# Kernel optimization log

Measured on AMD Instinct MI355X. Metric: run time of the kernel, lower is better.

The kernel has to match this reference:

```python
import jax, jax.numpy as jnp
import numpy as np

N_NODES = 100000
N_EDGES = 600000
F_IN, HID, CLS = 128, 128, 16


def sage_conv(x, src, dst, W_l, b_l, W_r, n_nodes):
    # mean aggregation of neighbor features: message x[src] scattered to dst
    msg = x[src]                                              # [E, F]
    agg = jax.ops.segment_sum(msg, dst, num_segments=n_nodes)  # [N, F]
    deg = jax.ops.segment_sum(jnp.ones((src.shape[0],), x.dtype), dst, num_segments=n_nodes)
    agg = agg / jnp.maximum(deg, 1.0)[:, None]
    # PyG SAGEConv: lin_l(agg) (with bias) + lin_r(x_root) (no bias)
    return agg @ W_l + b_l + x @ W_r


def setup_inputs() -> dict:
    key = jax.random.key(0)
    ks = jax.random.split(key, 6)
    x = jax.random.normal(ks[0], (N_NODES, F_IN), jnp.float32)
    edge_index = jax.random.randint(ks[1], (2, N_EDGES), 0, N_NODES, dtype=jnp.int64)
    s1 = 1.0 / np.sqrt(F_IN)
    s2 = 1.0 / np.sqrt(HID)
    return {
        "x": x,
        "edge_index": edge_index,
        "W1_l": jax.random.normal(ks[2], (F_IN, HID), jnp.float32) * s1,
        "b1": jnp.zeros((HID,), jnp.float32),
        "W1_r": jax.random.normal(ks[3], (F_IN, HID), jnp.float32) * s1,
        "W2_l": jax.random.normal(ks[4], (HID, CLS), jnp.float32) * s2,
        "b2": jnp.zeros((CLS,), jnp.float32),
        "W2_r": jax.random.normal(ks[5], (HID, CLS), jnp.float32) * s2,
    }


def reference(x, edge_index, W1_l, b1, W1_r, W2_l, b2, W2_r):
    n = x.shape[0]
    src, dst = edge_index[0], edge_index[1]
    h = sage_conv(x, src, dst, W1_l, b1, W1_r, n)
    h = jax.nn.relu(h)
    # F.dropout(training=self.training): identity in eval mode
    out = sage_conv(h, src, dst, W2_l, b2, W2_r, n)
    return jax.nn.log_softmax(out, axis=1)
```

## Files before the change

### kernel.cpp

```cpp
#include <hip/hip_runtime.h>
#include <cstdint>

#define N_NODES 100000
#define N_PAD 100096
#define N_EDGES 600000
#define F 128
#define CLS 16
#define CAP 32

typedef short bf16x8 __attribute__((ext_vector_type(8)));
typedef float f32x4 __attribute__((ext_vector_type(4)));

__device__ inline float bf2f(unsigned int lo16) { return __uint_as_float(lo16 << 16); }
__device__ inline unsigned short f2b(float f) {
    unsigned int u = __float_as_uint(f);
    return (unsigned short)((u + 0x7fffu + ((u >> 16) & 1u)) >> 16);
}

__global__ __launch_bounds__(256) void init_k(int* __restrict__ deg,
                                              const float* __restrict__ x,
                                              unsigned short* __restrict__ xb,
                                              const float* __restrict__ W1l,
                                              const float* __restrict__ W1r,
                                              const float* __restrict__ W2l,
                                              const float* __restrict__ W2r,
                                              unsigned short* __restrict__ w1t,
                                              unsigned short* __restrict__ w2t) {
    int b = blockIdx.x;
    if (b < 98) {
        int i = b * 1024 + threadIdx.x * 4;
#pragma unroll
        for (int k = 0; k < 4; k++)
            if (i + k < N_NODES) deg[i + k] = 0;
    } else if (b < 12598) {
        int i = (b - 98) * 256 + threadIdx.x;
        if (i < N_NODES * F / 4) {
            float4 v = ((const float4*)x)[i];
            ushort4 o;
            o.x = f2b(v.x); o.y = f2b(v.y); o.z = f2b(v.z); o.w = f2b(v.w);
            ((ushort4*)xb)[i] = o;
        }
    } else if (b < 12726) {
        int idx = (b - 12598) * 256 + threadIdx.x;
        int n = idx >> 8, k = idx & 255;
        float v = (k < F) ? W1l[k * F + n] : W1r[(k - F) * F + n];
        int ct = n >> 4, m = n & 15;
        int half = k >> 7, ks = (k >> 5) & 3, quad = (k >> 3) & 3, j = k & 7;
        w1t[(ct * 8 + ks * 2 + half) * 512 + (quad * 16 + m) * 8 + j] = f2b(v);
    } else {
        int idx = (b - 12726) * 256 + threadIdx.x;
        if (idx < 32 * F) {
            int n = idx >> 7, k = idx & 127;
            float v = (n < CLS) ? W2l[k * CLS + n] : W2r[k * CLS + (n - CLS)];
            int tile = n >> 4, m = n & 15;
            int ks = (k >> 5) & 3, quad = (k >> 3) & 3, j = k & 7;
            w2t[(tile * 4 + ks) * 512 + (quad * 16 + m) * 8 + j] = f2b(v);
        }
    }
}

__global__ void fill_k(const int* __restrict__ src, const int* __restrict__ dst,
                       int* __restrict__ deg, int* __restrict__ bucket) {
    int e = blockIdx.x * blockDim.x + threadIdx.x;
    if (e < N_EDGES) {
        int d = dst[e];
        int slot = atomicAdd(&deg[d], 1);
        if (slot < CAP) bucket[d * CAP + slot] = src[e];
    }
}

__global__ __launch_bounds__(256) void gemm_fused(const unsigned short* __restrict__ Xb,
                                                  const int* __restrict__ deg,
                                                  const int* __restrict__ bucket,
                                                  const unsigned short* __restrict__ Wt,
                                                  const float* __restrict__ bias,
                                                  const unsigned short* __restrict__ Wt2,
                                                  unsigned short* __restrict__ trLb,
                                                  float* __restrict__ trR) {
    __shared__ unsigned short sh[128 * 136];
    int tid = threadIdx.x;
    int row0 = blockIdx.x * 128;

    {
        int ns = tid >> 1, half = tid & 1;
        const int4* gsrc = (const int4*)(bucket + (size_t)(row0 + ns) * CAP + half * 16);
        int* drow = (int*)(sh + ns * 136);
        int4* ldst = (int4*)(drow + half * 16);
        ldst[0] = gsrc[0];
        ldst[1] = gsrc[1];
        ldst[2] = gsrc[2];
        ldst[3] = gsrc[3];
        if (half == 0) drow[32] = deg[row0 + ns];
    }

    int grp = tid >> 4, l16 = tid & 15, f8 = l16 * 8;
    int lrb = grp * 8;

#define ISSUE(P, DV, LR) do { \
    const int* brow_ = (const int*)(sh + (LR) * 136); \
    int node_ = row0 + (LR); \
    int draw_ = brow_[32]; \
    DV = (node_ < N_NODES) ? min(max(draw_, 0), CAP) : 0; \
    int4 b0_ = ((const int4*)brow_)[0]; \
    int4 b1_ = ((const int4*)brow_)[1]; \
    int4 b2_ = ((const int4*)brow_)[2]; \
    int n0_  = (DV > 0 ) ? min(max(b0_.x, 0), N_NODES - 1) : 0; \
    int n1_  = (DV > 1 ) ? min(max(b0_.y, 0), N_NODES - 1) : 0; \
    int n2_  = (DV > 2 ) ? min(max(b0_.z, 0), N_NODES - 1) : 0; \
    int n3_  = (DV > 3 ) ? min(max(b0_.w, 0), N_NODES - 1) : 0; \
    int n4_  = (DV > 4 ) ? min(max(b1_.x, 0), N_NODES - 1) : 0; \
    int n5_  = (DV > 5 ) ? min(max(b1_.y, 0), N_NODES - 1) : 0; \
    int n6_  = (DV > 6 ) ? min(max(b1_.z, 0), N_NODES - 1) : 0; \
    int n7_  = (DV > 7 ) ? min(max(b1_.w, 0), N_NODES - 1) : 0; \
    int n8_  = (DV > 8 ) ? min(max(b2_.x, 0), N_NODES - 1) : 0; \
    int n9_  = (DV > 9 ) ? min(max(b2_.y, 0), N_NODES - 1) : 0; \
    int n10_ = (DV > 10) ? min(max(b2_.z, 0), N_NODES - 1) : 0; \
    int n11_ = (DV > 11) ? min(max(b2_.w, 0), N_NODES - 1) : 0; \
    P##0  = *(const uint4*)(Xb + (size_t)n0_  * F + f8); \
    P##1  = *(const uint4*)(Xb + (size_t)n1_  * F + f8); \
    P##2  = *(const uint4*)(Xb + (size_t)n2_  * F + f8); \
    P##3  = *(const uint4*)(Xb + (size_t)n3_  * F + f8); \
    P##4  = *(const uint4*)(Xb + (size_t)n4_  * F + f8); \
    P##5  = *(const uint4*)(Xb + (size_t)n5_  * F + f8); \
    P##6  = *(const uint4*)(Xb + (size_t)n6_  * F + f8); \
    P##7  = *(const uint4*)(Xb + (size_t)n7_  * F + f8); \
    P##8  = *(const uint4*)(Xb + (size_t)n8_  * F + f8); \
    P##9  = *(const uint4*)(Xb + (size_t)n9_  * F + f8); \
    P##10 = *(const uint4*)(Xb + (size_t)n10_ * F + f8); \
    P##11 = *(const uint4*)(Xb + (size_t)n11_ * F + f8); \
} while (0)

#define ACC8(vv) { \
    acc_[0] += bf2f((vv).x & 0xffffu); acc_[1] += bf2f((vv).x >> 16); \
    acc_[2] += bf2f((vv).y & 0xffffu); acc_[3] += bf2f((vv).y >> 16); \
    acc_[4] += bf2f((vv).z & 0xffffu); acc_[5] += bf2f((vv).z >> 16); \
    acc_[6] += bf2f((vv).w & 0xffffu); acc_[7] += bf2f((vv).w >> 16); }

#define CONSUME(P, DV, LR) do { \
    float acc_[8] = {0.f, 0.f, 0.f, 0.f, 0.f, 0.f, 0.f, 0.f}; \
    if (DV > 0)  ACC8(P##0); \
    if (DV > 1)  ACC8(P##1); \
    if (DV > 2)  ACC8(P##2); \
    if (DV > 3)  ACC8(P##3); \
    if (DV > 4)  ACC8(P##4); \
    if (DV > 5)  ACC8(P##5); \
    if (DV > 6)  ACC8(P##6); \
    if (DV > 7)  ACC8(P##7); \
    if (DV > 8)  ACC8(P##8); \
    if (DV > 9)  ACC8(P##9); \
    if (DV > 10) ACC8(P##10); \
    if (DV > 11) ACC8(P##11); \
    if (DV > 12) { \
        const int* brow_ = (const int*)(sh + (LR) * 136); \
        for (int j0 = 12; j0 < DV; j0 += 4) { \
            int4 bb_ = *(const int4*)(brow_ + j0); \
            int rem_ = DV - j0; \
            int m0_ = (rem_ > 0) ? min(max(bb_.x, 0), N_NODES - 1) : 0; \
            int m1_ = (rem_ > 1) ? min(max(bb_.y, 0), N_NODES - 1) : 0; \
            int m2_ = (rem_ > 2) ? min(max(bb_.z, 0), N_NODES - 1) : 0; \
            int m3_ = (rem_ > 3) ? min(max(bb_.w, 0), N_NODES - 1) : 0; \
            uint4 w0_ = *(const uint4*)(Xb + (size_t)m0_ * F + f8); \
            uint4 w1_ = *(const uint4*)(Xb + (size_t)m1_ * F + f8); \
            uint4 w2_ = *(const uint4*)(Xb + (size_t)m2_ * F + f8); \
            uint4 w3_ = *(const uint4*)(Xb + (size_t)m3_ * F + f8); \
            if (rem_ > 0) ACC8(w0_); \
            if (rem_ > 1) ACC8(w1_); \
            if (rem_ > 2) ACC8(w2_); \
            if (rem_ > 3) ACC8(w3_); \
        } \
    } \
    float inv_ = 1.0f / fmaxf((float)DV, 1.0f); \
    uint4 o_; \
    o_.x = (unsigned int)f2b(acc_[0] * inv_) | ((unsigned int)f2b(acc_[1] * inv_) << 16); \
    o_.y = (unsigned int)f2b(acc_[2] * inv_) | ((unsigned int)f2b(acc_[3] * inv_) << 16); \
    o_.z = (unsigned int)f2b(acc_[4] * inv_) | ((unsigned int)f2b(acc_[5] * inv_) << 16); \
    o_.w = (unsigned int)f2b(acc_[6] * inv_) | ((unsigned int)f2b(acc_[7] * inv_) << 16); \
    *(uint4*)&sh[(LR) * 136 + f8] = o_; \
} while (0)

    {
        uint4 vA0, vA1, vA2, vA3, vA4, vA5, vA6, vA7, vA8, vA9, vA10, vA11;
        uint4 vB0, vB1, vB2, vB3, vB4, vB5, vB6, vB7, vB8, vB9, vB10, vB11;
        int dA, dB;
        ISSUE(vA, dA, lrb + 0);
        ISSUE(vB, dB, lrb + 1);
        CONSUME(vA, dA, lrb + 0);
        ISSUE(vA, dA, lrb + 2);
        CONSUME(vB, dB, lrb + 1);
        ISSUE(vB, dB, lrb + 3);
        CONSUME(vA, dA, lrb + 2);
        ISSUE(vA, dA, lrb + 4);
        CONSUME(vB, dB, lrb + 3);
        ISSUE(vB, dB, lrb + 5);
        CONSUME(vA, dA, lrb + 4);
        ISSUE(vA, dA, lrb + 6);
        CONSUME(vB, dB, lrb + 5);
        ISSUE(vB, dB, lrb + 7);
        CONSUME(vA, dA, lrb + 6);
        CONSUME(vB, dB, lrb + 7);
    }
#undef ISSUE
#undef ACC8
#undef CONSUME
    __syncthreads();

    int wave = tid >> 6, lane = tid & 63;
    int m = lane & 15, quad = lane >> 4;
    int koff = quad * 8;
    int wrow0 = row0 + wave * 32;

    const unsigned short* sa0 = sh + (wave * 32 + m) * 136 + koff;
    const unsigned short* sa1 = sa0 + 16 * 136;
    const unsigned short* px0 = Xb + (size_t)(wrow0 + m) * F + koff;
    const unsigned short* px1 = px0 + 16 * F;
    const unsigned short* pw = Wt + lane * 8;

    f32x4 acc0[8], acc1[8];
#pragma unroll
    for (int ct = 0; ct < 8; ct++) { acc0[ct] = (f32x4){0,0,0,0}; acc1[ct] = (f32x4){0,0,0,0}; }

#pragma unroll
    for (int ks = 0; ks < 4; ks++) {
        bf16x8 a0 = *(const bf16x8*)(const void*)(sa0 + ks * 32);
        bf16x8 a1 = *(const bf16x8*)(const void*)(sa1 + ks * 32);
        bf16x8 x0 = *(const bf16x8*)(const void*)(px0 + ks * 32);
        bf16x8 x1 = *(const bf16x8*)(const void*)(px1 + ks * 32);
#pragma unroll
        for (int ct = 0; ct < 8; ct++) {
            bf16x8 bl = *(const bf16x8*)(const void*)(pw + (ct * 8 + ks * 2 + 0) * 512);
            bf16x8 br = *(const bf16x8*)(const void*)(pw + (ct * 8 + ks * 2 + 1) * 512);
            acc0[ct] = __builtin_amdgcn_mfma_f32_16x16x32_bf16(a0, bl, acc0[ct], 0, 0, 0);
            acc1[ct] = __builtin_amdgcn_mfma_f32_16x16x32_bf16(a1, bl, acc1[ct], 0, 0, 0);
            acc0[ct] = __builtin_amdgcn_mfma_f32_16x16x32_bf16(x0, br, acc0[ct], 0, 0, 0);
            acc1[ct] = __builtin_amdgcn_mfma_f32_16x16x32_bf16(x1, br, acc1[ct], 0, 0, 0);
        }
    }
    __syncthreads();

    int lr0 = wave * 32 + quad * 4;
#pragma unroll
    for (int ct = 0; ct < 8; ct++) {
        int n = ct * 16 + m;
        float bv = bias[n];
#pragma unroll
        for (int r = 0; r < 4; r++) {
            sh[(lr0 + r) * 136 + n]      = f2b(fmaxf(acc0[ct][r] + bv, 0.f));
            sh[(lr0 + 16 + r) * 136 + n] = f2b(fmaxf(acc1[ct][r] + bv, 0.f));
        }
    }
    __syncthreads();

    const unsigned short* hl0 = sh + (wave * 32 + m) * 136 + koff;
    const unsigned short* hl1 = hl0 + 16 * 136;
    const unsigned short* pw2 = Wt2 + lane * 8;

    f32x4 al0 = (f32x4){0,0,0,0}, al1 = (f32x4){0,0,0,0};
    f32x4 ar0 = (f32x4){0,0,0,0}, ar1 = (f32x4){0,0,0,0};
#pragma unroll
    for (int ks = 0; ks < 4; ks++) {
        bf16x8 h0 = *(const bf16x8*)(const void*)(hl0 + ks * 32);
        bf16x8 h1 = *(const bf16x8*)(const void*)(hl1 + ks * 32);
        bf16x8 wl = *(const bf16x8*)(const void*)(pw2 + (0 * 4 + ks) * 512);
        bf16x8 wr = *(const bf16x8*)(const void*)(pw2 + (1 * 4 + ks) * 512);
        al0 = __builtin_amdgcn_mfma_f32_16x16x32_bf16(h0, wl, al0, 0, 0, 0);
        al1 = __builtin_amdgcn_mfma_f32_16x16x32_bf16(h1, wl, al1, 0, 0, 0);
        ar0 = __builtin_amdgcn_mfma_f32_16x16x32_bf16(h0, wr, ar0, 0, 0, 0);
        ar1 = __builtin_amdgcn_mfma_f32_16x16x32_bf16(h1, wr, ar1, 0, 0, 0);
    }
    int r0 = wrow0 + quad * 4;
#pragma unroll
    for (int r = 0; r < 4; r++) {
        trLb[(size_t)(r0 + r) * CLS + m]      = f2b(al0[r]);
        trLb[(size_t)(r0 + 16 + r) * CLS + m] = f2b(al1[r]);
        trR[(size_t)(r0 + r) * CLS + m]       = ar0[r];
        trR[(size_t)(r0 + 16 + r) * CLS + m]  = ar1[r];
    }
}

__global__ __launch_bounds__(256) void agg2sm_k(const unsigned short* __restrict__ trLb,
                                                const float* __restrict__ trR,
                                                const int* __restrict__ deg,
                                                const int* __restrict__ bucket,
                                                const float* __restrict__ b2,
                                                float* __restrict__ out) {
    int node = blockIdx.x * 4 + (threadIdx.x >> 6);
    int lane = threadIdx.x & 63;
    int r = lane >> 2;
    int cq = (lane & 3) * 4;
    const int* bk = bucket + node * CAP;

    int d_raw = deg[node];
    int d = min(d_raw, CAP);
    int nb = (r < d) ? min(max(bk[r], 0), N_NODES - 1) : 0;
    uint2 v = *(const uint2*)(trLb + (size_t)nb * CLS + cq);
    float4 selfR = *(const float4*)(trR + (size_t)node * CLS + cq);

    float4 acc = {0.f, 0.f, 0.f, 0.f};
    if (r < d) {
        acc.x += bf2f(v.x & 0xffffu); acc.y += bf2f(v.x >> 16);
        acc.z += bf2f(v.y & 0xffffu); acc.w += bf2f(v.y >> 16);
    }
    if (d > 16) {
        int idx = 16 + r;
        bool valid = idx < d;
        int m2 = valid ? min(max(bk[idx], 0), N_NODES - 1) : 0;
        uint2 w = *(const uint2*)(trLb + (size_t)m2 * CLS + cq);
        if (valid) {
            acc.x += bf2f(w.x & 0xffffu); acc.y += bf2f(w.x >> 16);
            acc.z += bf2f(w.y & 0xffffu); acc.w += bf2f(w.y >> 16);
        }
    }
#pragma unroll
    for (int off = 4; off <= 32; off <<= 1) {
        acc.x += __shfl_xor(acc.x, off);
        acc.y += __shfl_xor(acc.y, off);
        acc.z += __shfl_xor(acc.z, off);
        acc.w += __shfl_xor(acc.w, off);
    }
    float inv = 1.0f / fmaxf((float)d, 1.0f);
    float4 bb = *(const float4*)(b2 + cq);
    float vx = acc.x * inv + selfR.x + bb.x;
    float vy = acc.y * inv + selfR.y + bb.y;
    float vz = acc.z * inv + selfR.z + bb.z;
    float vw = acc.w * inv + selfR.w + bb.w;
    float mx = fmaxf(fmaxf(vx, vy), fmaxf(vz, vw));
    mx = fmaxf(mx, __shfl_xor(mx, 1));
    mx = fmaxf(mx, __shfl_xor(mx, 2));
    float sm = __expf(vx - mx) + __expf(vy - mx) + __expf(vz - mx) + __expf(vw - mx);
    sm += __shfl_xor(sm, 1);
    sm += __shfl_xor(sm, 2);
    float lg = __logf(sm);
    if (r == 0) {
        float4 o = {vx - mx - lg, vy - mx - lg, vz - mx - lg, vw - mx - lg};
        *(float4*)(out + (size_t)node * CLS + cq) = o;
    }
}


extern "C" void kernel_launch(void* const* d_in, const int* in_sizes, int n_in,
                              void* d_out, int out_size, void* d_ws, size_t ws_size,
                              hipStream_t stream) {
    const float* x   = (const float*)d_in[0];
    const int*   ei  = (const int*)d_in[1];
    const float* W1l = (const float*)d_in[2];
    const float* b1  = (const float*)d_in[3];
    const float* W1r = (const float*)d_in[4];
    const float* W2l = (const float*)d_in[5];
    const float* b2  = (const float*)d_in[6];
    const float* W2r = (const float*)d_in[7];
    float* out = (float*)d_out;

    const int* src = ei;
    const int* dst = ei + N_EDGES;

    char* ws = (char*)d_ws;
    size_t off = 0;
    auto alloc = [&](size_t bytes) { char* p = ws + off; off += (bytes + 127) / 128 * 128; return p; };
    int* deg    = (int*)alloc((size_t)N_NODES * 4);
    int* bucket = (int*)alloc((size_t)N_NODES * CAP * 4);
    unsigned short* xb   = (unsigned short*)alloc((size_t)N_PAD * F * 2);
    unsigned short* trLb = (unsigned short*)alloc((size_t)N_PAD * CLS * 2);
    float*          trR  = (float*)alloc((size_t)N_PAD * CLS * 4);
    unsigned short* w1t  = (unsigned short*)alloc((size_t)F * 256 * 2);
    unsigned short* w2t  = (unsigned short*)alloc((size_t)32 * F * 2);

    init_k<<<12743, 256, 0, stream>>>(deg, x, xb, W1l, W1r, W2l, W2r, w1t, w2t);
    fill_k<<<(N_EDGES + 255) / 256, 256, 0, stream>>>(src, dst, deg, bucket);
    gemm_fused<<<N_PAD / 128, 256, 0, stream>>>(xb, deg, bucket, w1t, b1, w2t, trLb, trR);
    agg2sm_k<<<N_NODES / 4, 256, 0, stream>>>(trLb, trR, deg, bucket, b2, out);
}
```

Measured before the change: 211.1 us.

## Fuse edge bucketing into prep kernel and narrow gather lanes to 4 features

Moves degree zeroing to a memset and merges the edge bucket-fill kernel with the bf16 conversion and weight-packing kernel, which removes one kernel launch and lets the atomics overlap with the conversion work. In the fused GEMM's neighbour-mean gather, each thread now handles 4 features with 8-byte loads instead of 8 features with 16-byte loads, so 32 threads cover a row and each group processes 16 rows in a rolled loop. This is meant to lower register pressure and raise occupancy, at the cost of more, smaller gather transactions. The x conversion branch also drops its bounds check, which relies on the block count exactly covering the array.

New measurement: 218.6 us. 3.6% more time.

```diff
diff --git a/kernel.cpp b/kernel.cpp
--- a/kernel.cpp
+++ b/kernel.cpp
@@ -17,7 +17,10 @@
     return (unsigned short)((u + 0x7fffu + ((u >> 16) & 1u)) >> 16);
 }
 
-__global__ __launch_bounds__(256) void init_k(int* __restrict__ deg,
+__global__ __launch_bounds__(256) void prep_k(const int* __restrict__ src,
+                                              const int* __restrict__ dst,
+                                              int* __restrict__ deg,
+                                              int* __restrict__ bucket,
                                               const float* __restrict__ x,
                                               unsigned short* __restrict__ xb,
                                               const float* __restrict__ W1l,
@@ -27,28 +30,28 @@
                                               unsigned short* __restrict__ w1t,
                                               unsigned short* __restrict__ w2t) {
     int b = blockIdx.x;
-    if (b < 98) {
-        int i = b * 1024 + threadIdx.x * 4;
-#pragma unroll
-        for (int k = 0; k < 4; k++)
-            if (i + k < N_NODES) deg[i + k] = 0;
-    } else if (b < 12598) {
-        int i = (b - 98) * 256 + threadIdx.x;
-        if (i < N_NODES * F / 4) {
-            float4 v = ((const float4*)x)[i];
-            ushort4 o;
-            o.x = f2b(v.x); o.y = f2b(v.y); o.z = f2b(v.z); o.w = f2b(v.w);
-            ((ushort4*)xb)[i] = o;
-        }
-    } else if (b < 12726) {
-        int idx = (b - 12598) * 256 + threadIdx.x;
+    if (b < 2344) {
+        int e = b * 256 + threadIdx.x;
+        if (e < N_EDGES) {
+            int d = dst[e];
+            int slot = atomicAdd(&deg[d], 1);
+            if (slot < CAP) bucket[d * CAP + slot] = src[e];
+        }
+    } else if (b < 14844) {
+        int i = (b - 2344) * 256 + threadIdx.x;
+        float4 v = ((const float4*)x)[i];
+        ushort4 o;
+        o.x = f2b(v.x); o.y = f2b(v.y); o.z = f2b(v.z); o.w = f2b(v.w);
+        ((ushort4*)xb)[i] = o;
+    } else if (b < 14972) {
+        int idx = (b - 14844) * 256 + threadIdx.x;
         int n = idx >> 8, k = idx & 255;
         float v = (k < F) ? W1l[k * F + n] : W1r[(k - F) * F + n];
         int ct = n >> 4, m = n & 15;
         int half = k >> 7, ks = (k >> 5) & 3, quad = (k >> 3) & 3, j = k & 7;
         w1t[(ct * 8 + ks * 2 + half) * 512 + (quad * 16 + m) * 8 + j] = f2b(v);
     } else {
-        int idx = (b - 12726) * 256 + threadIdx.x;
+        int idx = (b - 14972) * 256 + threadIdx.x;
         if (idx < 32 * F) {
             int n = idx >> 7, k = idx & 127;
             float v = (n < CLS) ? W2l[k * CLS + n] : W2r[k * CLS + (n - CLS)];
@@ -56,16 +59,6 @@
             int ks = (k >> 5) & 3, quad = (k >> 3) & 3, j = k & 7;
             w2t[(tile * 4 + ks) * 512 + (quad * 16 + m) * 8 + j] = f2b(v);
         }
-    }
-}
-
-__global__ void fill_k(const int* __restrict__ src, const int* __restrict__ dst,
-                       int* __restrict__ deg, int* __restrict__ bucket) {
-    int e = blockIdx.x * blockDim.x + threadIdx.x;
-    if (e < N_EDGES) {
-        int d = dst[e];
-        int slot = atomicAdd(&deg[d], 1);
-        if (slot < CAP) bucket[d * CAP + slot] = src[e];
     }
 }
 
@@ -93,8 +86,8 @@
         if (half == 0) drow[32] = deg[row0 + ns];
     }
 
-    int grp = tid >> 4, l16 = tid & 15, f8 = l16 * 8;
-    int lrb = grp * 8;
+    int grp = tid >> 5, c4 = (tid & 31) * 4;
+    int lrb = grp * 16;
 
 #define ISSUE(P, DV, LR) do { \
     const int* brow_ = (const int*)(sh + (LR) * 136); \
@@ -116,40 +109,38 @@
     int n9_  = (DV > 9 ) ? min(max(b2_.y, 0), N_NODES - 1) : 0; \
     int n10_ = (DV > 10) ? min(max(b2_.z, 0), N_NODES - 1) : 0; \
     int n11_ = (DV > 11) ? min(max(b2_.w, 0), N_NODES - 1) : 0; \
-    P##0  = *(const uint4*)(Xb + (size_t)n0_  * F + f8); \
-    P##1  = *(const uint4*)(Xb + (size_t)n1_  * F + f8); \
-    P##2  = *(const uint4*)(Xb + (size_t)n2_  * F + f8); \
-    P##3  = *(const uint4*)(Xb + (size_t)n3_  * F + f8); \
-    P##4  = *(const uint4*)(Xb + (size_t)n4_  * F + f8); \
-    P##5  = *(const uint4*)(Xb + (size_t)n5_  * F + f8); \
-    P##6  = *(const uint4*)(Xb + (size_t)n6_  * F + f8); \
-    P##7  = *(const uint4*)(Xb + (size_t)n7_  * F + f8); \
-    P##8  = *(const uint4*)(Xb + (size_t)n8_  * F + f8); \
-    P##9  = *(const uint4*)(Xb + (size_t)n9_  * F + f8); \
-    P##10 = *(const uint4*)(Xb + (size_t)n10_ * F + f8); \
-    P##11 = *(const uint4*)(Xb + (size_t)n11_ * F + f8); \
+    P##0  = *(const uint2*)(Xb + (size_t)n0_  * F + c4); \
+    P##1  = *(const uint2*)(Xb + (size_t)n1_  * F + c4); \
+    P##2  = *(const uint2*)(Xb + (size_t)n2_  * F + c4); \
+    P##3  = *(const uint2*)(Xb + (size_t)n3_  * F + c4); \
+    P##4  = *(const uint2*)(Xb + (size_t)n4_  * F + c4); \
+    P##5  = *(const uint2*)(Xb + (size_t)n5_  * F + c4); \
+    P##6  = *(const uint2*)(Xb + (size_t)n6_  * F + c4); \
+    P##7  = *(const uint2*)(Xb + (size_t)n7_  * F + c4); \
+    P##8  = *(const uint2*)(Xb + (size_t)n8_  * F + c4); \
+    P##9  = *(const uint2*)(Xb + (size_t)n9_  * F + c4); \
+    P##10 = *(const uint2*)(Xb + (size_t)n10_ * F + c4); \
+    P##11 = *(const uint2*)(Xb + (size_t)n11_ * F + c4); \
 } while (0)
 
-#define ACC8(vv) { \
+#define ACC4(vv) { \
     acc_[0] += bf2f((vv).x & 0xffffu); acc_[1] += bf2f((vv).x >> 16); \
-    acc_[2] += bf2f((vv).y & 0xffffu); acc_[3] += bf2f((vv).y >> 16); \
-    acc_[4] += bf2f((vv).z & 0xffffu); acc_[5] += bf2f((vv).z >> 16); \
-    acc_[6] += bf2f((vv).w & 0xffffu); acc_[7] += bf2f((vv).w >> 16); }
+    acc_[2] += bf2f((vv).y & 0xffffu); acc_[3] += bf2f((vv).y >> 16); }
 
 #define CONSUME(P, DV, LR) do { \
-    float acc_[8] = {0.f, 0.f, 0.f, 0.f, 0.f, 0.f, 0.f, 0.f}; \
-    if (DV > 0)  ACC8(P##0); \
-    if (DV > 1)  ACC8(P##1); \
-    if (DV > 2)  ACC8(P##2); \
-    if (DV > 3)  ACC8(P##3); \
-    if (DV > 4)  ACC8(P##4); \
-    if (DV > 5)  ACC8(P##5); \
-    if (DV > 6)  ACC8(P##6); \
-    if (DV > 7)  ACC8(P##7); \
-    if (DV > 8)  ACC8(P##8); \
-    if (DV > 9)  ACC8(P##9); \
-    if (DV > 10) ACC8(P##10); \
-    if (DV > 11) ACC8(P##11); \
+    float acc_[4] = {0.f, 0.f, 0.f, 0.f}; \
+    if (DV > 0)  ACC4(P##0); \
+    if (DV > 1)  ACC4(P##1); \
+    if (DV > 2)  ACC4(P##2); \
+    if (DV > 3)  ACC4(P##3); \
+    if (DV > 4)  ACC4(P##4); \
+    if (DV > 5)  ACC4(P##5); \
+    if (DV > 6)  ACC4(P##6); \
+    if (DV > 7)  ACC4(P##7); \
+    if (DV > 8)  ACC4(P##8); \
+    if (DV > 9)  ACC4(P##9); \
+    if (DV > 10) ACC4(P##10); \
+    if (DV > 11) ACC4(P##11); \
     if (DV > 12) { \
         const int* brow_ = (const int*)(sh + (LR) * 136); \
         for (int j0 = 12; j0 < DV; j0 += 4) { \
@@ -159,48 +150,41 @@
             int m1_ = (rem_ > 1) ? min(max(bb_.y, 0), N_NODES - 1) : 0; \
             int m2_ = (rem_ > 2) ? min(max(bb_.z, 0), N_NODES - 1) : 0; \
             int m3_ = (rem_ > 3) ? min(max(bb_.w, 0), N_NODES - 1) : 0; \
-            uint4 w0_ = *(const uint4*)(Xb + (size_t)m0_ * F + f8); \
-            uint4 w1_ = *(const uint4*)(Xb + (size_t)m1_ * F + f8); \
-            uint4 w2_ = *(const uint4*)(Xb + (size_t)m2_ * F + f8); \
-            uint4 w3_ = *(const uint4*)(Xb + (size_t)m3_ * F + f8); \
-            if (rem_ > 0) ACC8(w0_); \
-            if (rem_ > 1) ACC8(w1_); \
-            if (rem_ > 2) ACC8(w2_); \
-            if (rem_ > 3) ACC8(w3_); \
+            uint2 w0_ = *(const uint2*)(Xb + (size_t)m0_ * F + c4); \
+            uint2 w1_ = *(const uint2*)(Xb + (size_t)m1_ * F + c4); \
+            uint2 w2_ = *(const uint2*)(Xb + (size_t)m2_ * F + c4); \
+            uint2 w3_ = *(const uint2*)(Xb + (size_t)m3_ * F + c4); \
+            if (rem_ > 0) ACC4(w0_); \
+            if (rem_ > 1) ACC4(w1_); \
+            if (rem_ > 2) ACC4(w2_); \
+            if (rem_ > 3) ACC4(w3_); \
         } \
     } \
     float inv_ = 1.0f / fmaxf((float)DV, 1.0f); \
-    uint4 o_; \
+    uint2 o_; \
     o_.x = (unsigned int)f2b(acc_[0] * inv_) | ((unsigned int)f2b(acc_[1] * inv_) << 16); \
     o_.y = (unsigned int)f2b(acc_[2] * inv_) | ((unsigned int)f2b(acc_[3] * inv_) << 16); \
-    o_.z = (unsigned int)f2b(acc_[4] * inv_) | ((unsigned int)f2b(acc_[5] * inv_) << 16); \
-    o_.w = (unsigned int)f2b(acc_[6] * inv_) | ((unsigned int)f2b(acc_[7] * inv_) << 16); \
-    *(uint4*)&sh[(LR) * 136 + f8] = o_; \
+    *(uint2*)&sh[(LR) * 136 + c4] = o_; \
 } while (0)
 
     {
-        uint4 vA0, vA1, vA2, vA3, vA4, vA5, vA6, vA7, vA8, vA9, vA10, vA11;
-        uint4 vB0, vB1, vB2, vB3, vB4, vB5, vB6, vB7, vB8, vB9, vB10, vB11;
+        uint2 vA0, vA1, vA2, vA3, vA4, vA5, vA6, vA7, vA8, vA9, vA10, vA11;
+        uint2 vB0, vB1, vB2, vB3, vB4, vB5, vB6, vB7, vB8, vB9, vB10, vB11;
         int dA, dB;
         ISSUE(vA, dA, lrb + 0);
         ISSUE(vB, dB, lrb + 1);
-        CONSUME(vA, dA, lrb + 0);
-        ISSUE(vA, dA, lrb + 2);
-        CONSUME(vB, dB, lrb + 1);
-        ISSUE(vB, dB, lrb + 3);
-        CONSUME(vA, dA, lrb + 2);
-        ISSUE(vA, dA, lrb + 4);
-        CONSUME(vB, dB, lrb + 3);
-        ISSUE(vB, dB, lrb + 5);
-        CONSUME(vA, dA, lrb + 4);
-        ISSUE(vA, dA, lrb + 6);
-        CONSUME(vB, dB, lrb + 5);
-        ISSUE(vB, dB, lrb + 7);
-        CONSUME(vA, dA, lrb + 6);
-        CONSUME(vB, dB, lrb + 7);
+#pragma unroll 1
+        for (int rr = 0; rr < 14; rr += 2) {
+            CONSUME(vA, dA, lrb + rr);
+            ISSUE(vA, dA, lrb + rr + 2);
+            CONSUME(vB, dB, lrb + rr + 1);
+            ISSUE(vB, dB, lrb + rr + 3);
+        }
+        CONSUME(vA, dA, lrb + 14);
+        CONSUME(vB, dB, lrb + 15);
     }
 #undef ISSUE
-#undef ACC8
+#undef ACC4
 #undef CONSUME
     __syncthreads();
 
@@ -364,8 +348,9 @@
     unsigned short* w1t  = (unsigned short*)alloc((size_t)F * 256 * 2);
     unsigned short* w2t  = (unsigned short*)alloc((size_t)32 * F * 2);
 
-    init_k<<<12743, 256, 0, stream>>>(deg, x, xb, W1l, W1r, W2l, W2r, w1t, w2t);
-    fill_k<<<(N_EDGES + 255) / 256, 256, 0, stream>>>(src, dst, deg, bucket);
+    hipMemsetAsync(deg, 0, (size_t)N_NODES * 4, stream);
+    prep_k<<<14988, 256, 0, stream>>>(src, dst, deg, bucket, x, xb,
+                                      W1l, W1r, W2l, W2r, w1t, w2t);
     gemm_fused<<<N_PAD / 128, 256, 0, stream>>>(xb, deg, bucket, w1t, b1, w2t, trLb, trR);
     agg2sm_k<<<N_NODES / 4, 256, 0, stream>>>(trLb, trR, deg, bucket, b2, out);
 }
```
